# Optimization experiments

Measured on AMD Instinct MI355X. Metric: run time of the kernel, lower is better.

Reference implementation:

```python
import jax, jax.numpy as jnp
import numpy as np

B, SQ, SK, D, H = 8, 2048, 2048, 512, 8
QP, KP, VP = 512, 512, 4096  # VP must equal D*H for O_w to accept the concat


def setup_inputs() -> dict:
    key = jax.random.key(0)
    ks = jax.random.split(key, 9)
    q_in = jax.random.normal(ks[0], (B, SQ, D), dtype=jnp.float32)
    k_in = jax.random.normal(ks[1], (B, SK, D), dtype=jnp.float32)
    v_in = jax.random.normal(ks[2], (B, SK, D), dtype=jnp.float32)
    mask = jax.random.randint(ks[3], (B, SQ, SK), 0, 2, dtype=jnp.int32)
    W_q = jax.random.normal(ks[4], (D, QP), dtype=jnp.float32) * 0.02
    W_k = jax.random.normal(ks[5], (D, KP), dtype=jnp.float32) * 0.02
    W_v = jax.random.normal(ks[6], (D, VP), dtype=jnp.float32) * 0.02
    W_o = jax.random.normal(ks[7], (VP, D), dtype=jnp.float32) * 0.02
    b_o = jnp.zeros((D,), dtype=jnp.float32)
    return {"q_in": q_in, "k_in": k_in, "v_in": v_in,
            "W_q": W_q, "W_k": W_k, "W_v": W_v, "W_o": W_o, "b_o": b_o,
            "mask": mask}


def reference(q_in, k_in, v_in, W_q, W_k, W_v, W_o, b_o, mask):
    b, sq, d = q_in.shape
    sk = k_in.shape[1]
    # NOTE: original scales by sqrt(input_dim // num_heads), NOT actual head dim
    scale = jnp.asarray(np.sqrt(d // H), dtype=q_in.dtype)
    q = q_in @ W_q  # (B, Sq, QP)
    k = k_in @ W_k  # (B, Sk, KP)
    v = v_in @ W_v  # (B, Sk, VP)
    q_h = q.reshape(b, sq, H, -1).transpose(0, 2, 1, 3)  # (B,H,Sq,dq)
    k_h = k.reshape(b, sk, H, -1).transpose(0, 2, 1, 3)  # (B,H,Sk,dk)
    v_h = v.reshape(b, sk, H, -1).transpose(0, 2, 1, 3)  # (B,H,Sk,dv)
    attn = jnp.einsum('bhid,bhkd->bhik', q_h, k_h)  # (B,H,Sq,Sk)
    attn = jnp.where(mask[:, None, :, :] == 0, jnp.asarray(-1e9, attn.dtype), attn)
    attn = jax.nn.softmax(attn / scale, axis=-1)
    out = attn @ v_h  # (B,H,Sq,dv)
    # Faithful to original bug: transpose(0,1) swaps BATCH and HEAD, then reshape
    out = jnp.transpose(out, (1, 0, 2, 3)).reshape(b, sq, -1)  # (B,Sq,H*dv)
    return out @ W_o + b_o
```

## Files before the change

kernel.cpp:

```cpp
#include <hip/hip_runtime.h>
#include <math.h>

typedef __bf16 bf16x8 __attribute__((ext_vector_type(8)));
typedef float fx4 __attribute__((ext_vector_type(4)));
typedef unsigned short u16;
typedef unsigned short u16x8 __attribute__((ext_vector_type(8)));
typedef unsigned int u32;
typedef unsigned char u8;

__device__ __forceinline__ fx4 mfma16(bf16x8 a, bf16x8 b, fx4 c) {
  return __builtin_amdgcn_mfma_f32_16x16x32_bf16(a, b, c, 0, 0, 0);
}
__device__ __forceinline__ u16 f2bf(float f) {
  u32 u = __float_as_uint(f);
  u += 0x7fffu + ((u >> 16) & 1u);
  return (u16)(u >> 16);
}
__device__ __forceinline__ u16 bfc(float f) {
  __bf16 h = (__bf16)f;
  return __builtin_bit_cast(u16, h);
}
__device__ __forceinline__ float ex2(float x) { return __builtin_amdgcn_exp2f(x); }

#define BB 8
#define SS 2048
#define DD 512
#define HH 8
#define DQ 64
#define DV 512
#define VP 4096

#define OFF_QP  ((size_t)0)
#define OFF_KP  ((size_t)16777216)
#define OFF_WQT ((size_t)33554432)
#define OFF_WKT ((size_t)34078720)
#define OFF_WVT ((size_t)34603008)
#define OFF_WOT ((size_t)38797312)
#define OFF_MB  ((size_t)42991616)
#define OFF_VT  ((size_t)76546048)
#define OFF_XB  ((size_t)210763776)

__global__ __launch_bounds__(256) void transpose_w(const float* __restrict__ W,
                                                   u16* __restrict__ Wt,
                                                   int K, int N) {
  __shared__ float t[32][33];
  const int n0 = blockIdx.x * 32, k0 = blockIdx.y * 32;
  const int tx = threadIdx.x & 31, ty = threadIdx.x >> 5;
#pragma unroll
  for (int i = 0; i < 32; i += 8)
    t[ty + i][tx] = W[(size_t)(k0 + ty + i) * N + n0 + tx];
  __syncthreads();
#pragma unroll
  for (int i = 0; i < 32; i += 8)
    Wt[(size_t)(n0 + ty + i) * K + k0 + tx] = f2bf(t[tx][ty + i]);
}

__global__ __launch_bounds__(256) void mask_packbits(const int* __restrict__ m,
                                                     u32* __restrict__ mb) {
  const size_t widx = (size_t)blockIdx.x * 256 + threadIdx.x;
  const int* src = m + widx * 32;
  u32 r = 0;
#pragma unroll
  for (int j = 0; j < 32; j += 4) {
    int4 a = *(const int4*)(src + j);
    r |= (a.x ? 1u : 0u) << j;
    r |= (a.y ? 1u : 0u) << (j + 1);
    r |= (a.z ? 1u : 0u) << (j + 2);
    r |= (a.w ? 1u : 0u) << (j + 3);
  }
  mb[widx] = r;
}

template <int AFP32, int EPI>
__global__ __launch_bounds__(256) void gemm_bt(const void* __restrict__ Ap,
                                               const u16* __restrict__ Bt,
                                               void* __restrict__ Cp,
                                               int M, int N, int K,
                                               const float* __restrict__ bias,
                                               float scale) {
  __shared__ union {
    struct { u16 As[128 * 32]; u16 Bs[128 * 32]; } s;
    u16 T[4][64 * 68];
  } sm;
  const int tid = threadIdx.x;
  const int lane = tid & 63, w = tid >> 6;
  const int lhi = lane >> 4, llo = lane & 15;
  const int wm = w >> 1, wn = w & 1;
  const int m0 = blockIdx.y * 128, n0 = blockIdx.x * 128;

  fx4 acc[4][4];
#pragma unroll
  for (int i = 0; i < 4; ++i)
#pragma unroll
    for (int j = 0; j < 4; ++j) acc[i][j] = (fx4){0.f, 0.f, 0.f, 0.f};

  for (int k0 = 0; k0 < K; k0 += 32) {
    if (AFP32) {
      const float* A = (const float*)Ap;
      const int row = tid >> 1, co = (tid & 1) * 16;
      const float* src = A + (size_t)(m0 + row) * K + k0 + co;
      float4 v0 = *(const float4*)(src + 0);
      float4 v1 = *(const float4*)(src + 4);
      float4 v2 = *(const float4*)(src + 8);
      float4 v3 = *(const float4*)(src + 12);
      u16x8 p0 = {f2bf(v0.x), f2bf(v0.y), f2bf(v0.z), f2bf(v0.w),
                  f2bf(v1.x), f2bf(v1.y), f2bf(v1.z), f2bf(v1.w)};
      u16x8 p1 = {f2bf(v2.x), f2bf(v2.y), f2bf(v2.z), f2bf(v2.w),
                  f2bf(v3.x), f2bf(v3.y), f2bf(v3.z), f2bf(v3.w)};
      *(u16x8*)&sm.s.As[row * 32 + co] = p0;
      *(u16x8*)&sm.s.As[row * 32 + co + 8] = p1;
    } else {
      const u16* A = (const u16*)Ap;
#pragma unroll
      for (int j = 0; j < 2; ++j) {
        int cc = j * 256 + tid;
        int row = cc >> 2, c8 = (cc & 3) * 8;
        *(uint4*)&sm.s.As[cc * 8] = *(const uint4*)&A[(size_t)(m0 + row) * K + k0 + c8];
      }
    }
#pragma unroll
    for (int j = 0; j < 2; ++j) {
      int cc = j * 256 + tid;
      int row = cc >> 2, c8 = (cc & 3) * 8;
      *(uint4*)&sm.s.Bs[cc * 8] = *(const uint4*)&Bt[(size_t)(n0 + row) * K + k0 + c8];
    }
    __syncthreads();
    bf16x8 af[4], bfv[4];
#pragma unroll
    for (int mi = 0; mi < 4; ++mi)
      af[mi] = *(const bf16x8*)&sm.s.As[(wm * 64 + mi * 16 + llo) * 32 + lhi * 8];
#pragma unroll
    for (int ni = 0; ni < 4; ++ni)
      bfv[ni] = *(const bf16x8*)&sm.s.Bs[(wn * 64 + ni * 16 + llo) * 32 + lhi * 8];
#pragma unroll
    for (int mi = 0; mi < 4; ++mi)
#pragma unroll
      for (int ni = 0; ni < 4; ++ni)
        acc[mi][ni] = mfma16(af[mi], bfv[ni], acc[mi][ni]);
    __syncthreads();
  }

  const int rbase = m0 + wm * 64, cbase = n0 + wn * 64;
  if (EPI == 0) {
    u16* C = (u16*)Cp;
#pragma unroll
    for (int mi = 0; mi < 4; ++mi) {
      int r0 = rbase + mi * 16 + lhi * 4;
#pragma unroll
      for (int ni = 0; ni < 4; ++ni) {
        int c = cbase + ni * 16 + llo;
#pragma unroll
        for (int r = 0; r < 4; ++r)
          C[(size_t)(r0 + r) * N + c] = f2bf(acc[mi][ni][r] * scale);
      }
    }
  } else if (EPI == 1) {
    u16* Tw = &sm.T[w][0];
#pragma unroll
    for (int mi = 0; mi < 4; ++mi)
#pragma unroll
      for (int ni = 0; ni < 4; ++ni) {
        ushort4 pk;
        pk.x = f2bf(acc[mi][ni][0]);
        pk.y = f2bf(acc[mi][ni][1]);
        pk.z = f2bf(acc[mi][ni][2]);
        pk.w = f2bf(acc[mi][ni][3]);
        *(ushort4*)&Tw[(ni * 16 + llo) * 68 + mi * 16 + lhi * 4] = pk;
      }
    u16* VtC = (u16*)Cp;
    const int bsel = rbase >> 11;
    const int sb = rbase & 2047;
    u16* dst = VtC + ((size_t)(bsel * VP + cbase + lane)) * SS + sb;
#pragma unroll
    for (int j = 0; j < 8; ++j) {
      u16x8 vv = *(u16x8*)&Tw[lane * 68 + j * 8];
      *(u16x8*)&dst[j * 8] = vv;
    }
  } else {
    float* C = (float*)Cp;
#pragma unroll
    for (int ni = 0; ni < 4; ++ni) {
      int c = cbase + ni * 16 + llo;
      float bv = bias[c];
#pragma unroll
      for (int mi = 0; mi < 4; ++mi) {
        int r0 = rbase + mi * 16 + lhi * 4;
#pragma unroll
        for (int r = 0; r < 4; ++r)
          C[(size_t)(r0 + r) * N + c] = acc[mi][ni][r] + bv;
      }
    }
  }
}

#define KB 128
__global__ __launch_bounds__(256, 2) void attn(const u16* __restrict__ Qp,
                                               const u16* __restrict__ Kp,
                                               const u16* __restrict__ Vt,
                                               const u32* __restrict__ mb,
                                               u16* __restrict__ Xb) {
  const int lin = blockIdx.x;
  const int xcd = lin & 7, idx = lin >> 3;
  const int chunk = idx >> 5, qt = idx & 31;
  const int b = chunk >> 1, dvh = chunk & 1, h = xcd;
  const int m0 = qt * 64;
  const int tid = threadIdx.x, w = tid >> 6, lane = tid & 63;
  const int lhi = lane >> 4, llo = lane & 15;

  __shared__ u16 Psm[2][4][64][40];
  __shared__ float sm_lw[4][64];
  __shared__ float sm_l[64];

  bf16x8 qf[4][2];
#pragma unroll
  for (int mt = 0; mt < 4; ++mt)
#pragma unroll
    for (int ks = 0; ks < 2; ++ks)
      qf[mt][ks] = *(const bf16x8*)&Qp[(size_t)(b * SS + m0 + mt * 16 + llo) * 512 +
                                       h * DQ + ks * 32 + lhi * 8];

  fx4 acc[4][4];
#pragma unroll
  for (int mt = 0; mt < 4; ++mt)
#pragma unroll
    for (int nt = 0; nt < 4; ++nt) acc[mt][nt] = (fx4){0.f, 0.f, 0.f, 0.f};
  float lp[4] = {0.f, 0.f, 0.f, 0.f};

  const size_t kbase = (size_t)(b * SS) * 512 + h * DQ + lhi * 8;
  const size_t vbase =
      (size_t)(b * VP + h * DV + dvh * 256 + w * 64 + llo) * SS + lhi * 8;
  const u32* mrowp[4];
#pragma unroll
  for (int mt = 0; mt < 4; ++mt)
    mrowp[mt] = mb + (size_t)(b * SS + m0 + mt * 16 + llo) * 64 + w;
  const u32 bm0 = 1u << (lhi * 4), bm1 = bm0 << 1, bm2 = bm0 << 2, bm3 = bm0 << 3;

  bf16x8 kf[2][2];
  u32 mvc[4];
  bf16x8 vf[4][4];
#pragma unroll
  for (int st = 0; st < 2; ++st)
#pragma unroll
    for (int ks = 0; ks < 2; ++ks)
      kf[st][ks] = *(const bf16x8*)&Kp[kbase +
                                       (size_t)(w * 32 + st * 16 + llo) * 512 +
                                       ks * 32];
#pragma unroll
  for (int mt = 0; mt < 4; ++mt) mvc[mt] = mrowp[mt][0];
#pragma unroll
  for (int kk = 0; kk < 4; ++kk)
#pragma unroll
    for (int nt = 0; nt < 4; ++nt)
      vf[kk][nt] = *(const bf16x8*)&Vt[vbase + (size_t)(nt * 16) * SS + kk * 32];

  for (int n0 = 0; n0 < SS; n0 += KB) {
    const int buf = (n0 >> 7) & 1;
    const int nn = (n0 + KB) & (SS - 1);

#pragma unroll
    for (int mt = 0; mt < 4; ++mt) {
      const int qL = mt * 16 + llo;
      u16* Pw = &Psm[buf][w][qL][0];
#pragma unroll
      for (int st = 0; st < 2; ++st) {
        fx4 s = (fx4){0.f, 0.f, 0.f, 0.f};
        s = mfma16(kf[st][0], qf[mt][0], s);
        s = mfma16(kf[st][1], qf[mt][1], s);
        const u32 mst = mvc[mt] >> (st * 16);
        float p0 = (mst & bm0) ? ex2(s[0]) : 0.f;
        float p1 = (mst & bm1) ? ex2(s[1]) : 0.f;
        float p2 = (mst & bm2) ? ex2(s[2]) : 0.f;
        float p3 = (mst & bm3) ? ex2(s[3]) : 0.f;
        lp[mt] += (p0 + p1) + (p2 + p3);
        ushort4 pk = {bfc(p0), bfc(p1), bfc(p2), bfc(p3)};
        *(ushort4*)&Pw[st * 16 + lhi * 4] = pk;
      }
    }

    asm volatile("s_waitcnt lgkmcnt(0)" ::: "memory");
    __builtin_amdgcn_s_barrier();
    __builtin_amdgcn_sched_barrier(0);

#pragma unroll
    for (int st = 0; st < 2; ++st)
#pragma unroll
      for (int ks = 0; ks < 2; ++ks)
        kf[st][ks] = *(const bf16x8*)&Kp[kbase +
                                         (size_t)(nn + w * 32 + st * 16 + llo) * 512 +
                                         ks * 32];
#pragma unroll
    for (int mt = 0; mt < 4; ++mt) mvc[mt] = mrowp[mt][nn >> 5];

    const u16* Pb = &Psm[buf][0][0][0];
#pragma unroll
    for (int kk = 0; kk < 4; ++kk) {
      bf16x8 pf[4];
#pragma unroll
      for (int mt = 0; mt < 4; ++mt)
        pf[mt] = *(const bf16x8*)&Pb[(size_t)(kk * 64 + mt * 16 + llo) * 40 + lhi * 8];
      __builtin_amdgcn_s_setprio(1);
#pragma unroll
      for (int nt = 0; nt < 4; ++nt)
#pragma unroll
        for (int mt = 0; mt < 4; ++mt)
          acc[mt][nt] = mfma16(pf[mt], vf[kk][nt], acc[mt][nt]);
      __builtin_amdgcn_s_setprio(0);
    }

#pragma unroll
    for (int kk = 0; kk < 4; ++kk)
#pragma unroll
      for (int nt = 0; nt < 4; ++nt)
        vf[kk][nt] = *(const bf16x8*)&Vt[vbase + (size_t)(nt * 16) * SS + nn + kk * 32];
  }

#pragma unroll
  for (int mt = 0; mt < 4; ++mt) {
    lp[mt] += __shfl_xor(lp[mt], 16);
    lp[mt] += __shfl_xor(lp[mt], 32);
  }
  if (lhi == 0) {
#pragma unroll
    for (int mt = 0; mt < 4; ++mt) sm_lw[w][mt * 16 + llo] = lp[mt];
  }
  __syncthreads();
  if (tid < 64)
    sm_l[tid] = (sm_lw[0][tid] + sm_lw[1][tid]) + (sm_lw[2][tid] + sm_lw[3][tid]);
  __syncthreads();

  float linv[4][4];
#pragma unroll
  for (int mt = 0; mt < 4; ++mt)
#pragma unroll
    for (int r = 0; r < 4; ++r) linv[mt][r] = 1.0f / sm_l[mt * 16 + lhi * 4 + r];

  u16* Xs = &Psm[0][0][0][0];
  const int er = tid >> 4, ec = (tid & 15) * 16;
#pragma unroll
  for (int mt = 0; mt < 4; ++mt) {
#pragma unroll
    for (int nt = 0; nt < 4; ++nt)
#pragma unroll
      for (int r = 0; r < 4; ++r)
        Xs[(lhi * 4 + r) * 264 + w * 64 + nt * 16 + llo] =
            f2bf(acc[mt][nt][r] * linv[mt][r]);
    __syncthreads();
    {
      const u16* src = Xs + er * 264 + ec;
      u16* dst = Xb + (size_t)((h * 8 + b) * SS + m0 + mt * 16 + er) * 512 +
                 dvh * 256 + ec;
      uint4 a0 = *(const uint4*)(src + 0);
      uint4 a1 = *(const uint4*)(src + 8);
      *(uint4*)(dst + 0) = a0;
      *(uint4*)(dst + 8) = a1;
    }
    __syncthreads();
  }
}

extern "C" void kernel_launch(void* const* d_in, const int* in_sizes, int n_in,
                              void* d_out, int out_size, void* d_ws, size_t ws_size,
                              hipStream_t stream) {
  (void)in_sizes; (void)n_in; (void)out_size; (void)ws_size;
  const float* q_in = (const float*)d_in[0];
  const float* k_in = (const float*)d_in[1];
  const float* v_in = (const float*)d_in[2];
  const float* W_q  = (const float*)d_in[3];
  const float* W_k  = (const float*)d_in[4];
  const float* W_v  = (const float*)d_in[5];
  const float* W_o  = (const float*)d_in[6];
  const float* b_o  = (const float*)d_in[7];
  const int*   mask = (const int*)d_in[8];

  char* ws = (char*)d_ws;
  u16* Qp   = (u16*)(ws + OFF_QP);
  u16* Kp   = (u16*)(ws + OFF_KP);
  u16* Wqt  = (u16*)(ws + OFF_WQT);
  u16* Wkt  = (u16*)(ws + OFF_WKT);
  u16* Wvt  = (u16*)(ws + OFF_WVT);
  u16* Wot  = (u16*)(ws + OFF_WOT);
  u32* Mb   = (u32*)(ws + OFF_MB);
  u16* Vt   = (u16*)(ws + OFF_VT);
  u16* Xb   = (u16*)(ws + OFF_XB);

  transpose_w<<<dim3(16, 16), 256, 0, stream>>>(W_q, Wqt, 512, 512);
  transpose_w<<<dim3(16, 16), 256, 0, stream>>>(W_k, Wkt, 512, 512);
  transpose_w<<<dim3(128, 16), 256, 0, stream>>>(W_v, Wvt, 512, 4096);
  transpose_w<<<dim3(16, 128), 256, 0, stream>>>(W_o, Wot, 4096, 512);
  mask_packbits<<<dim3(4096), 256, 0, stream>>>(mask, Mb);

  gemm_bt<1, 0><<<dim3(4, 128), 256, 0, stream>>>(q_in, Wqt, Qp, 16384, 512, 512, nullptr, 0.18033688011112f);
  gemm_bt<1, 0><<<dim3(4, 128), 256, 0, stream>>>(k_in, Wkt, Kp, 16384, 512, 512, nullptr, 1.0f);
  gemm_bt<1, 1><<<dim3(32, 128), 256, 0, stream>>>(v_in, Wvt, Vt, 16384, 4096, 512, nullptr, 1.0f);

  attn<<<dim3(4096), 256, 0, stream>>>(Qp, Kp, Vt, Mb, Xb);

  gemm_bt<0, 2><<<dim3(4, 128), 256, 0, stream>>>(Xb, Wot, d_out, 16384, 512, 4096, b_o, 1.0f);
}
```

Measured before the change: 1.320 ms.

## Rewrite attention core with 32x32 MFMA and register-resident P via lane shuffles

```diff
diff --git a/kernel.cpp b/kernel.cpp
--- a/kernel.cpp
+++ b/kernel.cpp
@@ -3,24 +3,30 @@
 
 typedef __bf16 bf16x8 __attribute__((ext_vector_type(8)));
 typedef float fx4 __attribute__((ext_vector_type(4)));
+typedef float fx16 __attribute__((ext_vector_type(16)));
 typedef unsigned short u16;
 typedef unsigned short u16x8 __attribute__((ext_vector_type(8)));
 typedef unsigned int u32;
+typedef unsigned int u32x4 __attribute__((ext_vector_type(4)));
 typedef unsigned char u8;
 
 __device__ __forceinline__ fx4 mfma16(bf16x8 a, bf16x8 b, fx4 c) {
   return __builtin_amdgcn_mfma_f32_16x16x32_bf16(a, b, c, 0, 0, 0);
+}
+__device__ __forceinline__ fx16 mfma32(bf16x8 a, bf16x8 b, fx16 c) {
+  return __builtin_amdgcn_mfma_f32_32x32x16_bf16(a, b, c, 0, 0, 0);
 }
 __device__ __forceinline__ u16 f2bf(float f) {
   u32 u = __float_as_uint(f);
   u += 0x7fffu + ((u >> 16) & 1u);
   return (u16)(u >> 16);
 }
-__device__ __forceinline__ u16 bfc(float f) {
-  __bf16 h = (__bf16)f;
-  return __builtin_bit_cast(u16, h);
-}
 __device__ __forceinline__ float ex2(float x) { return __builtin_amdgcn_exp2f(x); }
+__device__ __forceinline__ u32 cvtpk(float lo, float hi) {
+  u32 r;
+  asm("v_cvt_pk_bf16_f32 %0, %1, %2" : "=v"(r) : "v"(lo), "v"(hi));
+  return r;
+}
 
 #define BB 8
 #define SS 2048
@@ -193,7 +199,65 @@
   }
 }
 
-#define KB 128
+#define Z16 {0.f,0.f,0.f,0.f,0.f,0.f,0.f,0.f,0.f,0.f,0.f,0.f,0.f,0.f,0.f,0.f}
+
+#define LOADK(S, KF, MW)                                                      \
+  do {                                                                        \
+    _Pragma("unroll") for (int ks = 0; ks < 4; ++ks)                          \
+        KF[ks] = *(const bf16x8*)&kb[(size_t)(S) * 512 + ks * 16];            \
+    MW = mbp[(S) >> 5];                                                       \
+  } while (0)
+
+#define LOADV(S)                                                              \
+  do {                                                                        \
+    _Pragma("unroll") for (int nt = 0; nt < 4; ++nt) {                        \
+      vf[nt][0] = *(const bf16x8*)&vb[nt][(S)];                               \
+      vf[nt][1] = *(const bf16x8*)&vb[nt][(S) + 16];                          \
+    }                                                                         \
+  } while (0)
+
+#define COMPUTE(KF, MW)                                                       \
+  do {                                                                        \
+    fx16 c = Z16;                                                             \
+    c = mfma32(KF[0], qf[0], c);                                              \
+    c = mfma32(KF[1], qf[1], c);                                              \
+    c = mfma32(KF[2], qf[2], c);                                              \
+    const u32 madj = (MW) >> (H * 4);                                         \
+    c = mfma32(KF[3], qf[3], c);                                              \
+    float p[16];                                                              \
+    _Pragma("unroll") for (int i = 0; i < 16; ++i) {                          \
+      const int bx = (i & 3) + 8 * (i >> 2);                                  \
+      float sv = (madj & (1u << bx)) ? c[i] : -1e9f;                          \
+      p[i] = ex2(sv);                                                         \
+    }                                                                         \
+    lp += ((((p[0] + p[1]) + (p[2] + p[3])) +                                 \
+            ((p[4] + p[5]) + (p[6] + p[7]))) +                                \
+           (((p[8] + p[9]) + (p[10] + p[11])) +                               \
+            ((p[12] + p[13]) + (p[14] + p[15]))));                            \
+    u32 pk[8];                                                                \
+    _Pragma("unroll") for (int j = 0; j < 8; ++j)                             \
+        pk[j] = cvtpk(p[2 * j], p[2 * j + 1]);                                \
+    bf16x8 pa[2];                                                             \
+    _Pragma("unroll") for (int k2 = 0; k2 < 2; ++k2) {                        \
+      u32 x0 = (u32)__shfl_xor((int)pk[4 * k2 + 0], 32);                      \
+      u32 x1 = (u32)__shfl_xor((int)pk[4 * k2 + 1], 32);                      \
+      u32 x2 = (u32)__shfl_xor((int)pk[4 * k2 + 2], 32);                      \
+      u32 x3 = (u32)__shfl_xor((int)pk[4 * k2 + 3], 32);                      \
+      u32x4 t;                                                                \
+      t.x = H ? x2 : pk[4 * k2 + 0];                                          \
+      t.y = H ? x3 : pk[4 * k2 + 1];                                          \
+      t.z = H ? pk[4 * k2 + 2] : x0;                                          \
+      t.w = H ? pk[4 * k2 + 3] : x1;                                          \
+      pa[k2] = __builtin_bit_cast(bf16x8, t);                                 \
+    }                                                                         \
+    __builtin_amdgcn_s_setprio(1);                                            \
+    _Pragma("unroll") for (int nt = 0; nt < 4; ++nt) {                        \
+      acc[nt] = mfma32(pa[0], vf[nt][0], acc[nt]);                            \
+      acc[nt] = mfma32(pa[1], vf[nt][1], acc[nt]);                            \
+    }                                                                         \
+    __builtin_amdgcn_s_setprio(0);                                            \
+  } while (0)
+
 __global__ __launch_bounds__(256, 2) void attn(const u16* __restrict__ Qp,
                                                const u16* __restrict__ Kp,
                                                const u16* __restrict__ Vt,
@@ -205,156 +269,61 @@
   const int b = chunk >> 1, dvh = chunk & 1, h = xcd;
   const int m0 = qt * 64;
   const int tid = threadIdx.x, w = tid >> 6, lane = tid & 63;
-  const int lhi = lane >> 4, llo = lane & 15;
-
-  __shared__ u16 Psm[2][4][64][40];
-  __shared__ float sm_lw[4][64];
-  __shared__ float sm_l[64];
-
-  bf16x8 qf[4][2];
-#pragma unroll
-  for (int mt = 0; mt < 4; ++mt)
-#pragma unroll
-    for (int ks = 0; ks < 2; ++ks)
-      qf[mt][ks] = *(const bf16x8*)&Qp[(size_t)(b * SS + m0 + mt * 16 + llo) * 512 +
-                                       h * DQ + ks * 32 + lhi * 8];
-
-  fx4 acc[4][4];
-#pragma unroll
-  for (int mt = 0; mt < 4; ++mt)
-#pragma unroll
-    for (int nt = 0; nt < 4; ++nt) acc[mt][nt] = (fx4){0.f, 0.f, 0.f, 0.f};
-  float lp[4] = {0.f, 0.f, 0.f, 0.f};
-
-  const size_t kbase = (size_t)(b * SS) * 512 + h * DQ + lhi * 8;
-  const size_t vbase =
-      (size_t)(b * VP + h * DV + dvh * 256 + w * 64 + llo) * SS + lhi * 8;
-  const u32* mrowp[4];
-#pragma unroll
-  for (int mt = 0; mt < 4; ++mt)
-    mrowp[mt] = mb + (size_t)(b * SS + m0 + mt * 16 + llo) * 64 + w;
-  const u32 bm0 = 1u << (lhi * 4), bm1 = bm0 << 1, bm2 = bm0 << 2, bm3 = bm0 << 3;
-
-  bf16x8 kf[2][2];
-  u32 mvc[4];
-  bf16x8 vf[4][4];
-#pragma unroll
-  for (int st = 0; st < 2; ++st)
-#pragma unroll
-    for (int ks = 0; ks < 2; ++ks)
-      kf[st][ks] = *(const bf16x8*)&Kp[kbase +
-                                       (size_t)(w * 32 + st * 16 + llo) * 512 +
-                                       ks * 32];
-#pragma unroll
-  for (int mt = 0; mt < 4; ++mt) mvc[mt] = mrowp[mt][0];
-#pragma unroll
-  for (int kk = 0; kk < 4; ++kk)
+  const int wq = w & 1, wd = w >> 1;
+  const int l31 = lane & 31, H = lane >> 5;
+
+  __shared__ float sml[4][32];
+
+  const int qrow = b * SS + m0 + wq * 32 + l31;
+
+  bf16x8 qf[4];
+#pragma unroll
+  for (int ks = 0; ks < 4; ++ks)
+    qf[ks] = *(const bf16x8*)&Qp[(size_t)qrow * 512 + h * DQ + ks * 16 + H * 8];
+
+  fx16 acc[4];
+#pragma unroll
+  for (int nt = 0; nt < 4; ++nt) acc[nt] = (fx16)Z16;
+  float lp = 0.f;
+
+  const u16* kb = Kp + (size_t)(b * SS + l31) * 512 + h * DQ + H * 8;
+  const u32* mbp = mb + (size_t)qrow * 64;
+  const u16* vb[4];
+#pragma unroll
+  for (int nt = 0; nt < 4; ++nt)
+    vb[nt] = Vt +
+             (size_t)(b * VP + h * DV + dvh * 256 + wd * 128 + nt * 32 + l31) * SS +
+             H * 8;
+
+  bf16x8 kf0[4], kf1[4], vf[4][2];
+  u32 mw0, mw1;
+  LOADK(0, kf0, mw0);
+
+#pragma unroll 1
+  for (int s0 = 0; s0 < SS; s0 += 64) {
+    LOADV(s0);
+    LOADK(s0 + 32, kf1, mw1);
+    COMPUTE(kf0, mw0);
+    LOADV(s0 + 32);
+    const int sn = (s0 + 64) & (SS - 1);
+    LOADK(sn, kf0, mw0);
+    COMPUTE(kf1, mw1);
+  }
+
+  lp += __shfl_xor(lp, 32);
+  if (H == 0) sml[w][l31] = lp;
+  float linv[16];
+#pragma unroll
+  for (int r = 0; r < 16; ++r)
+    linv[r] = 1.0f / sml[w][(r & 3) + 8 * (r >> 2) + 4 * H];
+
+#pragma unroll
+  for (int r = 0; r < 16; ++r) {
+    const int q = m0 + wq * 32 + (r & 3) + 8 * (r >> 2) + 4 * H;
+    u16* dst = Xb + (size_t)((h * 8 + b) * SS + q) * 512 + dvh * 256 + wd * 128 + l31;
 #pragma unroll
     for (int nt = 0; nt < 4; ++nt)
-      vf[kk][nt] = *(const bf16x8*)&Vt[vbase + (size_t)(nt * 16) * SS + kk * 32];
-
-  for (int n0 = 0; n0 < SS; n0 += KB) {
-    const int buf = (n0 >> 7) & 1;
-    const int nn = (n0 + KB) & (SS - 1);
-
-#pragma unroll
-    for (int mt = 0; mt < 4; ++mt) {
-      const int qL = mt * 16 + llo;
-      u16* Pw = &Psm[buf][w][qL][0];
-#pragma unroll
-      for (int st = 0; st < 2; ++st) {
-        fx4 s = (fx4){0.f, 0.f, 0.f, 0.f};
-        s = mfma16(kf[st][0], qf[mt][0], s);
-        s = mfma16(kf[st][1], qf[mt][1], s);
-        const u32 mst = mvc[mt] >> (st * 16);
-        float p0 = (mst & bm0) ? ex2(s[0]) : 0.f;
-        float p1 = (mst & bm1) ? ex2(s[1]) : 0.f;
-        float p2 = (mst & bm2) ? ex2(s[2]) : 0.f;
-        float p3 = (mst & bm3) ? ex2(s[3]) : 0.f;
-        lp[mt] += (p0 + p1) + (p2 + p3);
-        ushort4 pk = {bfc(p0), bfc(p1), bfc(p2), bfc(p3)};
-        *(ushort4*)&Pw[st * 16 + lhi * 4] = pk;
-      }
-    }
-
-    asm volatile("s_waitcnt lgkmcnt(0)" ::: "memory");
-    __builtin_amdgcn_s_barrier();
-    __builtin_amdgcn_sched_barrier(0);
-
-#pragma unroll
-    for (int st = 0; st < 2; ++st)
-#pragma unroll
-      for (int ks = 0; ks < 2; ++ks)
-        kf[st][ks] = *(const bf16x8*)&Kp[kbase +
-                                         (size_t)(nn + w * 32 + st * 16 + llo) * 512 +
-                                         ks * 32];
-#pragma unroll
-    for (int mt = 0; mt < 4; ++mt) mvc[mt] = mrowp[mt][nn >> 5];
-
-    const u16* Pb = &Psm[buf][0][0][0];
-#pragma unroll
-    for (int kk = 0; kk < 4; ++kk) {
-      bf16x8 pf[4];
-#pragma unroll
-      for (int mt = 0; mt < 4; ++mt)
-        pf[mt] = *(const bf16x8*)&Pb[(size_t)(kk * 64 + mt * 16 + llo) * 40 + lhi * 8];
-      __builtin_amdgcn_s_setprio(1);
-#pragma unroll
-      for (int nt = 0; nt < 4; ++nt)
-#pragma unroll
-        for (int mt = 0; mt < 4; ++mt)
-          acc[mt][nt] = mfma16(pf[mt], vf[kk][nt], acc[mt][nt]);
-      __builtin_amdgcn_s_setprio(0);
-    }
-
-#pragma unroll
-    for (int kk = 0; kk < 4; ++kk)
-#pragma unroll
-      for (int nt = 0; nt < 4; ++nt)
-        vf[kk][nt] = *(const bf16x8*)&Vt[vbase + (size_t)(nt * 16) * SS + nn + kk * 32];
-  }
-
-#pragma unroll
-  for (int mt = 0; mt < 4; ++mt) {
-    lp[mt] += __shfl_xor(lp[mt], 16);
-    lp[mt] += __shfl_xor(lp[mt], 32);
-  }
-  if (lhi == 0) {
-#pragma unroll
-    for (int mt = 0; mt < 4; ++mt) sm_lw[w][mt * 16 + llo] = lp[mt];
-  }
-  __syncthreads();
-  if (tid < 64)
-    sm_l[tid] = (sm_lw[0][tid] + sm_lw[1][tid]) + (sm_lw[2][tid] + sm_lw[3][tid]);
-  __syncthreads();
-
-  float linv[4][4];
-#pragma unroll
-  for (int mt = 0; mt < 4; ++mt)
-#pragma unroll
-    for (int r = 0; r < 4; ++r) linv[mt][r] = 1.0f / sm_l[mt * 16 + lhi * 4 + r];
-
-  u16* Xs = &Psm[0][0][0][0];
-  const int er = tid >> 4, ec = (tid & 15) * 16;
-#pragma unroll
-  for (int mt = 0; mt < 4; ++mt) {
-#pragma unroll
-    for (int nt = 0; nt < 4; ++nt)
-#pragma unroll
-      for (int r = 0; r < 4; ++r)
-        Xs[(lhi * 4 + r) * 264 + w * 64 + nt * 16 + llo] =
-            f2bf(acc[mt][nt][r] * linv[mt][r]);
-    __syncthreads();
-    {
-      const u16* src = Xs + er * 264 + ec;
-      u16* dst = Xb + (size_t)((h * 8 + b) * SS + m0 + mt * 16 + er) * 512 +
-                 dvh * 256 + ec;
-      uint4 a0 = *(const uint4*)(src + 0);
-      uint4 a1 = *(const uint4*)(src + 8);
-      *(uint4*)(dst + 0) = a0;
-      *(uint4*)(dst + 8) = a1;
-    }
-    __syncthreads();
+      dst[nt * 32] = f2bf(acc[nt][r] * linv[r]);
   }
 }
 
```

Result: slower. 2.089 ms (+58.3%).
